# Kernel tuning notes

Hardware: AMD Instinct MI355X
Metric: run time of the kernel (lower is better)

## Reference

```python
import jax, jax.numpy as jnp
import numpy as np

V, D, H, L, T_CTX = 50257, 768, 12, 12, 1024
HD = D // H
GELU_C = float(np.sqrt(2.0 / np.pi))


def new_gelu(x):
    return 0.5 * x * (1.0 + jnp.tanh(GELU_C * (x + 0.044715 * x ** 3)))


def layernorm(x, w, b, eps=1e-5):
    mu = jnp.mean(x, axis=-1, keepdims=True)
    var = jnp.var(x, axis=-1, keepdims=True)
    return (x - mu) * jax.lax.rsqrt(var + eps) * w + b


def setup_inputs() -> dict:
    key = jax.random.key(0)
    ks = jax.random.split(key, 20)
    B, T = 2, 1024
    s = 0.02
    inp = {
        "idx": jax.random.randint(ks[0], (B, T), 0, V),
        "targets": jax.random.randint(ks[1], (B, T), 0, V),
        "wte": jax.random.normal(ks[2], (V, D), jnp.float32) * s,
        "wpe": jax.random.normal(ks[3], (T_CTX, D), jnp.float32) * s,
        "ln1_w": jnp.ones((L, D)), "ln1_b": jnp.zeros((L, D)),
        "qkv_w": jax.random.normal(ks[4], (L, D, 3 * D), jnp.float32) * s,
        "qkv_b": jnp.zeros((L, 3 * D)),
        "proj_w": jax.random.normal(ks[5], (L, D, D), jnp.float32) * s,
        "proj_b": jnp.zeros((L, D)),
        "ln2_w": jnp.ones((L, D)), "ln2_b": jnp.zeros((L, D)),
        "fc_w": jax.random.normal(ks[6], (L, D, 4 * D), jnp.float32) * s,
        "fc_b": jnp.zeros((L, 4 * D)),
        "fc2_w": jax.random.normal(ks[7], (L, 4 * D, D), jnp.float32) * s,
        "fc2_b": jnp.zeros((L, D)),
        "lnf_w": jnp.ones((D,)), "lnf_b": jnp.zeros((D,)),
    }
    return inp


def _gpt_forward(idx, targets, wte, wpe, ln1_w, ln1_b, qkv_w, qkv_b, proj_w,
                 proj_b, ln2_w, ln2_b, fc_w, fc_b, fc2_w, fc2_b, lnf_w, lnf_b):
    B, T = idx.shape
    x = wte[idx] + wpe[:T]  # [B,T,D]
    scale = 1.0 / np.sqrt(HD)
    causal = jnp.tril(jnp.ones((T, T), dtype=bool))

    def block(x, p):
        l1w, l1b, qw, qb, pw, pb, l2w, l2b, fw, fb, f2w, f2b = p
        h = layernorm(x, l1w, l1b)
        qkv = h @ qw + qb  # [B,T,3D]
        q, k, v = jnp.split(qkv, 3, axis=-1)
        q = q.reshape(B, T, H, HD).transpose(0, 2, 1, 3)
        k = k.reshape(B, T, H, HD).transpose(0, 2, 1, 3)
        v = v.reshape(B, T, H, HD).transpose(0, 2, 1, 3)
        attn = jnp.einsum('bhqd,bhkd->bhqk', q, k) * scale
        attn = jnp.where(causal, attn, -jnp.inf)
        attn = jax.nn.softmax(attn, axis=-1)
        o = jnp.einsum('bhqk,bhkd->bhqd', attn, v)
        o = o.transpose(0, 2, 1, 3).reshape(B, T, D)
        x = x + (o @ pw + pb)
        h = layernorm(x, l2w, l2b)
        h = new_gelu(h @ fw + fb) @ f2w + f2b
        return x + h, None

    params = (ln1_w, ln1_b, qkv_w, qkv_b, proj_w, proj_b,
              ln2_w, ln2_b, fc_w, fc_b, fc2_w, fc2_b)
    x, _ = jax.lax.scan(block, x, params)
    x = layernorm(x, lnf_w, lnf_b)
    logits = x @ wte.T  # tied lm_head, [B,T,V]

    logp = jax.nn.log_softmax(logits, axis=-1)
    tflat = targets.reshape(-1)
    valid = tflat != -1
    tsafe = jnp.where(valid, tflat, 0)
    nll = -jnp.take_along_axis(logp.reshape(-1, V), tsafe[:, None], axis=-1)[:, 0]
    loss = jnp.sum(jnp.where(valid, nll, 0.0)) / jnp.maximum(jnp.sum(valid), 1)
    return logits, loss


def reference(idx, targets, wte, wpe, ln1_w, ln1_b, qkv_w, qkv_b, proj_w,
              proj_b, ln2_w, ln2_b, fc_w, fc_b, fc2_w, fc2_b, lnf_w, lnf_b):
    return _gpt_forward(idx, targets, wte, wpe, ln1_w, ln1_b, qkv_w, qkv_b,
                        proj_w, proj_b, ln2_w, ln2_b, fc_w, fc_b, fc2_w, fc2_b,
                        lnf_w, lnf_b)
```

## Files before the change

kernel.cpp:

```cpp
#include <hip/hip_runtime.h>
#include <hip/hip_bf16.h>
#include <math.h>

#define TT 1024
#define BB 2
#define DD 768
#define HH 12
#define NHD 64
#define LL 12
#define VV 50257
#define MROWS (BB*TT)
#define VPAD 50304
#define NT 393

typedef __attribute__((ext_vector_type(4))) float f32x4;
typedef __attribute__((ext_vector_type(8))) __bf16 bf16x8;
typedef __attribute__((ext_vector_type(8))) unsigned short u16x8;
typedef __hip_bfloat16 bf16;

__device__ __forceinline__ void gload_lds16(const bf16* g, bf16* l) {
    __builtin_amdgcn_global_load_lds((const __attribute__((address_space(1))) void*)g,
                                     (__attribute__((address_space(3))) void*)l, 16, 0, 0);
}

__global__ void embed_kernel(const int* __restrict__ idx, const float* __restrict__ wte,
                             const float* __restrict__ wpe, float* __restrict__ x) {
    int m = blockIdx.x;
    int t = m % TT;
    int tok = idx[m];
    const float* wrow = wte + (size_t)tok * DD;
    const float* prow = wpe + (size_t)t * DD;
    float* xrow = x + (size_t)m * DD;
    for (int c = threadIdx.x; c < DD; c += blockDim.x)
        xrow[c] = wrow[c] + prow[c];
}

__global__ void ln_kernel(const float* __restrict__ x, const float* __restrict__ w,
                          const float* __restrict__ b, bf16* __restrict__ out) {
    __shared__ float red[256];
    int m = blockIdx.x;
    int tid = threadIdx.x;
    const float* xr = x + (size_t)m * DD;
    float v0 = xr[tid], v1 = xr[tid + 256], v2 = xr[tid + 512];
    red[tid] = v0 + v1 + v2;
    __syncthreads();
    for (int s = 128; s > 0; s >>= 1) { if (tid < s) red[tid] += red[tid + s]; __syncthreads(); }
    float mu = red[0] * (1.0f / DD);
    __syncthreads();
    float d0 = v0 - mu, d1 = v1 - mu, d2 = v2 - mu;
    red[tid] = d0 * d0 + d1 * d1 + d2 * d2;
    __syncthreads();
    for (int s = 128; s > 0; s >>= 1) { if (tid < s) red[tid] += red[tid + s]; __syncthreads(); }
    float rstd = rsqrtf(red[0] * (1.0f / DD) + 1e-5f);
    bf16* orow = out + (size_t)m * DD;
    orow[tid]       = __float2bfloat16(d0 * rstd * w[tid]       + b[tid]);
    orow[tid + 256] = __float2bfloat16(d1 * rstd * w[tid + 256] + b[tid + 256]);
    orow[tid + 512] = __float2bfloat16(d2 * rstd * w[tid + 512] + b[tid + 512]);
}

__global__ void redln_kernel(const float* __restrict__ part, const float* __restrict__ bias,
                             const float* __restrict__ w, const float* __restrict__ b,
                             float* __restrict__ x, bf16* __restrict__ hb) {
    __shared__ float red[256];
    const size_t MN = (size_t)MROWS * DD;
    int m = blockIdx.x;
    int tid = threadIdx.x;
    float v[3];
    #pragma unroll
    for (int j = 0; j < 3; ++j) {
        int c = tid + j * 256;
        size_t i = (size_t)m * DD + c;
        v[j] = x[i] + part[i] + part[MN + i] + bias[c];
        x[i] = v[j];
    }
    red[tid] = v[0] + v[1] + v[2];
    __syncthreads();
    for (int s = 128; s > 0; s >>= 1) { if (tid < s) red[tid] += red[tid + s]; __syncthreads(); }
    float mu = red[0] * (1.0f / DD);
    __syncthreads();
    float d0 = v[0] - mu, d1 = v[1] - mu, d2 = v[2] - mu;
    red[tid] = d0 * d0 + d1 * d1 + d2 * d2;
    __syncthreads();
    for (int s = 128; s > 0; s >>= 1) { if (tid < s) red[tid] += red[tid + s]; __syncthreads(); }
    float rstd = rsqrtf(red[0] * (1.0f / DD) + 1e-5f);
    bf16* orow = hb + (size_t)m * DD;
    orow[tid]       = __float2bfloat16(d0 * rstd * w[tid]       + b[tid]);
    orow[tid + 256] = __float2bfloat16(d1 * rstd * w[tid + 256] + b[tid + 256]);
    orow[tid + 512] = __float2bfloat16(d2 * rstd * w[tid + 512] + b[tid + 512]);
}

__global__ void cast_kernel(const float* __restrict__ src, bf16* __restrict__ dst, int n4) {
    int stride = gridDim.x * blockDim.x;
    for (int i = blockIdx.x * blockDim.x + threadIdx.x; i < n4; i += stride) {
        float4 v = *(const float4*)(src + (size_t)i * 4);
        bf16* d = dst + (size_t)i * 4;
        d[0] = __float2bfloat16(v.x); d[1] = __float2bfloat16(v.y);
        d[2] = __float2bfloat16(v.z); d[3] = __float2bfloat16(v.w);
    }
}

__global__ void padzero_kernel(bf16* __restrict__ p, int n) {
    int i = blockIdx.x * 256 + threadIdx.x;
    if (i < n) p[i] = __float2bfloat16(0.f);
}

__global__ void tcast_kernel(const float* __restrict__ W, bf16* __restrict__ Wt,
                             int K, int N, size_t wstride, size_t tstride) {
    W  += (size_t)blockIdx.z * wstride;
    Wt += (size_t)blockIdx.z * tstride;
    __shared__ float t[32][33];
    int n0 = blockIdx.x * 32, k0 = blockIdx.y * 32;
    int c = threadIdx.x & 31, g = threadIdx.x >> 5;
    #pragma unroll
    for (int i = 0; i < 4; ++i) {
        int k = g * 4 + i;
        t[k][c] = W[(size_t)(k0 + k) * N + n0 + c];
    }
    __syncthreads();
    #pragma unroll
    for (int i = 0; i < 4; ++i) {
        int n = g * 4 + i;
        Wt[(size_t)(n0 + n) * K + k0 + c] = __float2bfloat16(t[c][n]);
    }
}

template<int BM, int BN, bool BIAS, bool GELU_, bool RES, bool OUTBF16, bool SPLITK>
__global__ __launch_bounds__(256, 3) void mgemm(
        const bf16* __restrict__ A, const bf16* __restrict__ Bm,
        const float* __restrict__ bias, const float* __restrict__ res,
        float* __restrict__ Cf, bf16* __restrict__ Cb, int M, int N, int K) {
    constexpr int WM = BM / 32, WN = BN / 32;
    constexpr int RA = BM / 64, RB = BN / 64;
    constexpr int NL = RA + RB;
    __shared__ __align__(16) bf16 As[2][BM * 32];
    __shared__ __align__(16) bf16 Bs[2][BN * 32];
    const int tid = threadIdx.x, lane = tid & 63, wid = tid >> 6;
    const int nbx = gridDim.x;
    const int nwg = nbx * gridDim.y;
    const int bidl = blockIdx.x + nbx * blockIdx.y;
    const int cpx = nwg >> 3;
    const int sw = (bidl & 7) * cpx + (bidl >> 3);
    const int m0 = (sw % nbx) * BM, n0 = (sw / nbx) * BN;
    const int wr = (wid >> 1) * (BM / 2), wc = (wid & 1) * (BN / 2);
    const int fr = lane & 15, fq = lane >> 4;

    const int Keff  = SPLITK ? (K >> 1) : K;
    const int kbase = SPLITK ? blockIdx.z * Keff : 0;
    if (SPLITK) Cf += (size_t)blockIdx.z * M * N;

    const int ksrc = ((lane & 3) ^ ((lane >> 3) & 3)) * 8;
    const bf16* gA = A  + (size_t)(m0 + wid * 16 + (lane >> 2)) * K + kbase + ksrc;
    const bf16* gB = Bm + (size_t)(n0 + wid * 16 + (lane >> 2)) * K + kbase + ksrc;
    bf16* lA = &As[0][0] + wid * 512 + lane * 8;
    bf16* lB = &Bs[0][0] + wid * 512 + lane * 8;
    const int kph = (fq ^ ((fr >> 1) & 3)) * 8;

    f32x4 acc[WM][WN] = {};
    const int nt = Keff / 32;

    #pragma unroll
    for (int i = 0; i < RA; ++i) gload_lds16(gA + (size_t)(i * 64) * K, lA + i * 2048);
    #pragma unroll
    for (int i = 0; i < RB; ++i) gload_lds16(gB + (size_t)(i * 64) * K, lB + i * 2048);

    for (int t = 0; t < nt; ++t) {
        const int cur = t & 1;
        if (t + 1 < nt) {
            const bf16* pA = gA + (t + 1) * 32;
            const bf16* pB = gB + (t + 1) * 32;
            bf16* dA = lA + (cur ^ 1) * (BM * 32);
            bf16* dB = lB + (cur ^ 1) * (BN * 32);
            #pragma unroll
            for (int i = 0; i < RA; ++i) gload_lds16(pA + (size_t)(i * 64) * K, dA + i * 2048);
            #pragma unroll
            for (int i = 0; i < RB; ++i) gload_lds16(pB + (size_t)(i * 64) * K, dB + i * 2048);
            asm volatile("s_waitcnt vmcnt(%0)" :: "i"(NL) : "memory");
        } else {
            asm volatile("s_waitcnt vmcnt(0)" ::: "memory");
        }
        __builtin_amdgcn_s_barrier();
        __builtin_amdgcn_sched_barrier(0);
        const bf16* abase = &As[cur][0];
        const bf16* bbase = &Bs[cur][0];
        bf16x8 af[WM], bq[WN];
        #pragma unroll
        for (int m = 0; m < WM; ++m)
            af[m] = *(const bf16x8*)(abase + (wr + m * 16 + fr) * 32 + kph);
        #pragma unroll
        for (int n = 0; n < WN; ++n)
            bq[n] = *(const bf16x8*)(bbase + (wc + n * 16 + fr) * 32 + kph);
        #pragma unroll
        for (int m = 0; m < WM; ++m)
            #pragma unroll
            for (int n = 0; n < WN; ++n)
                acc[m][n] = __builtin_amdgcn_mfma_f32_16x16x32_bf16(af[m], bq[n], acc[m][n], 0, 0, 0);
        __builtin_amdgcn_sched_barrier(0);
        __builtin_amdgcn_s_barrier();
    }

    #pragma unroll
    for (int m = 0; m < WM; ++m) {
        const int row = m0 + wr + m * 16 + fq * 4;
        #pragma unroll
        for (int n = 0; n < WN; ++n) {
            const int col = n0 + wc + n * 16 + fr;
            float bv = BIAS ? bias[col] : 0.f;
            #pragma unroll
            for (int r = 0; r < 4; ++r) {
                float v = acc[m][n][r] + bv;
                if (GELU_) {
                    float u = v;
                    float z = 1.5957691216057308f * (u + 0.044715f * u * u * u);
                    v = u / (1.0f + __expf(-z));
                }
                if (RES) v += res[(size_t)(row + r) * N + col];
                if (OUTBF16) Cb[(size_t)(row + r) * N + col] = __float2bfloat16(v);
                else         Cf[(size_t)(row + r) * N + col] = v;
            }
        }
    }
}

__global__ __launch_bounds__(256, 3) void mgemmL(
        const bf16* __restrict__ A, const bf16* __restrict__ Bm,
        float* __restrict__ Cf, float2* __restrict__ P, int N, int K) {
    constexpr int NL = 4;
    __shared__ __align__(16) bf16 As[2][128 * 32];
    __shared__ __align__(16) bf16 Bs[2][128 * 32];
    __shared__ float2 lbuf[4][64];
    const int tid = threadIdx.x, lane = tid & 63, wid = tid >> 6;
    const int nbx = gridDim.x;
    const int nwg = nbx * gridDim.y;
    const int bidl = blockIdx.x + nbx * blockIdx.y;
    const int cpx = nwg >> 3;
    const int sw = (bidl & 7) * cpx + (bidl >> 3);
    const int m0 = (sw % nbx) * 128, n0 = (sw / nbx) * 128;
    const int wr = (wid >> 1) * 64, wc = (wid & 1) * 64;
    const int fr = lane & 15, fq = lane >> 4;

    const int ksrc = ((lane & 3) ^ ((lane >> 3) & 3)) * 8;
    const bf16* gA = A  + (size_t)(m0 + wid * 16 + (lane >> 2)) * K + ksrc;
    const bf16* gB = Bm + (size_t)(n0 + wid * 16 + (lane >> 2)) * K + ksrc;
    bf16* lA = &As[0][0] + wid * 512 + lane * 8;
    bf16* lB = &Bs[0][0] + wid * 512 + lane * 8;
    const int kph = (fq ^ ((fr >> 1) & 3)) * 8;

    f32x4 acc[4][4] = {};
    const int nt = K / 32;

    #pragma unroll
    for (int i = 0; i < 2; ++i) gload_lds16(gA + (size_t)(i * 64) * K, lA + i * 2048);
    #pragma unroll
    for (int i = 0; i < 2; ++i) gload_lds16(gB + (size_t)(i * 64) * K, lB + i * 2048);

    for (int t = 0; t < nt; ++t) {
        const int cur = t & 1;
        if (t + 1 < nt) {
            const bf16* pA = gA + (t + 1) * 32;
            const bf16* pB = gB + (t + 1) * 32;
            bf16* dA = lA + (cur ^ 1) * (128 * 32);
            bf16* dB = lB + (cur ^ 1) * (128 * 32);
            #pragma unroll
            for (int i = 0; i < 2; ++i) gload_lds16(pA + (size_t)(i * 64) * K, dA + i * 2048);
            #pragma unroll
            for (int i = 0; i < 2; ++i) gload_lds16(pB + (size_t)(i * 64) * K, dB + i * 2048);
            asm volatile("s_waitcnt vmcnt(%0)" :: "i"(NL) : "memory");
        } else {
            asm volatile("s_waitcnt vmcnt(0)" ::: "memory");
        }
        __builtin_amdgcn_s_barrier();
        __builtin_amdgcn_sched_barrier(0);
        const bf16* abase = &As[cur][0];
        const bf16* bbase = &Bs[cur][0];
        bf16x8 af[4], bq[4];
        #pragma unroll
        for (int m = 0; m < 4; ++m)
            af[m] = *(const bf16x8*)(abase + (wr + m * 16 + fr) * 32 + kph);
        #pragma unroll
        for (int n = 0; n < 4; ++n)
            bq[n] = *(const bf16x8*)(bbase + (wc + n * 16 + fr) * 32 + kph);
        #pragma unroll
        for (int m = 0; m < 4; ++m)
            #pragma unroll
            for (int n = 0; n < 4; ++n)
                acc[m][n] = __builtin_amdgcn_mfma_f32_16x16x32_bf16(af[m], bq[n], acc[m][n], 0, 0, 0);
        __builtin_amdgcn_sched_barrier(0);
        __builtin_amdgcn_s_barrier();
    }

    #pragma unroll
    for (int m = 0; m < 4; ++m) {
        const int row = m0 + wr + m * 16 + fq * 4;
        #pragma unroll
        for (int n = 0; n < 4; ++n) {
            const int col = n0 + wc + n * 16 + fr;
            if (col < N) {
                #pragma unroll
                for (int r = 0; r < 4; ++r)
                    Cf[(size_t)(row + r) * N + col] = acc[m][n][r];
            }
        }
    }
    #pragma unroll
    for (int m = 0; m < 4; ++m) {
        #pragma unroll
        for (int r = 0; r < 4; ++r) {
            float mx = -1e30f;
            #pragma unroll
            for (int n = 0; n < 4; ++n) {
                int col = n0 + wc + n * 16 + fr;
                mx = fmaxf(mx, (col < N) ? acc[m][n][r] : -1e30f);
            }
            #pragma unroll
            for (int msk = 1; msk <= 8; msk <<= 1) mx = fmaxf(mx, __shfl_xor(mx, msk));
            float sm = 0.f;
            #pragma unroll
            for (int n = 0; n < 4; ++n) {
                int col = n0 + wc + n * 16 + fr;
                if (col < N) sm += __expf(acc[m][n][r] - mx);
            }
            #pragma unroll
            for (int msk = 1; msk <= 8; msk <<= 1) sm += __shfl_xor(sm, msk);
            if (fr == 0) lbuf[wid][m * 16 + fq * 4 + r] = make_float2(mx, sm);
        }
    }
    __syncthreads();
    if (tid < 128) {
        int half = tid >> 6, rl = tid & 63;
        float2 a = lbuf[half * 2][rl];
        float2 b = lbuf[half * 2 + 1][rl];
        float mc = fmaxf(a.x, b.x);
        float sc = a.y * __expf(a.x - mc) + b.y * __expf(b.x - mc);
        P[(size_t)(m0 + half * 64 + rl) * NT + (n0 >> 7)] = make_float2(mc, sc);
    }
}

__global__ __launch_bounds__(256) void attn3_kernel(const bf16* __restrict__ qkv,
                                                    bf16* __restrict__ out) {
    __shared__ bf16 Vt[64 * 64];
    __shared__ bf16 Ps[4][16 * 64];
    const int bid = blockIdx.x;
    const int q0 = (15 - (bid & 15)) * 64;
    const int h  = (bid / (TT / 64)) % HH;
    const int b  = bid / ((TT / 64) * HH);
    const int tid = threadIdx.x, lane = tid & 63, wid = tid >> 6;
    const int fr = lane & 15, fq = lane >> 4;
    const size_t rs = 3 * DD;

    bf16x8 qf[2];
    {
        const bf16* qb = qkv + (size_t)(b * TT + q0 + wid * 16 + fr) * rs + h * NHD;
        qf[0] = *(const bf16x8*)(qb + fq * 8);
        qf[1] = *(const bf16x8*)(qb + 32 + fq * 8);
    }
    float mrun[4] = {-1e30f, -1e30f, -1e30f, -1e30f};
    float lrun[4] = {0.f, 0.f, 0.f, 0.f};
    f32x4 o[4] = {};
    const int vrow = (tid & 31) * 2, kq = tid >> 5;
    const int ntile = q0 / 64 + 1;

    for (int jt = 0; jt < ntile; ++jt) {
        __syncthreads();
        {
            const u16x8* vb = (const u16x8*)(qkv + (size_t)(b * TT + jt * 64 + vrow) * rs + 2 * DD + h * NHD + kq * 8);
            u16x8 v0 = vb[0];
            u16x8 v1 = *(const u16x8*)((const bf16*)vb + rs);
            #pragma unroll
            for (int j = 0; j < 8; ++j) {
                int d = kq * 8 + j;
                int e = (d * 64 + vrow) ^ ((d & 7) << 3);
                *(unsigned int*)&Vt[e] = (unsigned int)v0[j] | ((unsigned int)v1[j] << 16);
            }
        }
        f32x4 s[4] = {};
        const bf16* kb = qkv + (size_t)(b * TT + jt * 64 + fr) * rs + DD + h * NHD;
        __builtin_amdgcn_s_setprio(1);
        #pragma unroll
        for (int n = 0; n < 4; ++n) {
            bf16x8 k0 = *(const bf16x8*)(kb + (size_t)(n * 16) * rs + fq * 8);
            bf16x8 k1 = *(const bf16x8*)(kb + (size_t)(n * 16) * rs + 32 + fq * 8);
            s[n] = __builtin_amdgcn_mfma_f32_16x16x32_bf16(qf[0], k0, s[n], 0, 0, 0);
            s[n] = __builtin_amdgcn_mfma_f32_16x16x32_bf16(qf[1], k1, s[n], 0, 0, 0);
        }
        __builtin_amdgcn_s_setprio(0);
        float mt[4] = {-1e30f, -1e30f, -1e30f, -1e30f};
        #pragma unroll
        for (int n = 0; n < 4; ++n) {
            int colg = jt * 64 + n * 16 + fr;
            #pragma unroll
            for (int r = 0; r < 4; ++r) {
                int rowg = q0 + wid * 16 + fq * 4 + r;
                float v = s[n][r] * 0.125f;
                if (colg > rowg) v = -1e30f;
                s[n][r] = v;
                mt[r] = fmaxf(mt[r], v);
            }
        }
        #pragma unroll
        for (int msk = 1; msk <= 8; msk <<= 1)
            #pragma unroll
            for (int r = 0; r < 4; ++r) mt[r] = fmaxf(mt[r], __shfl_xor(mt[r], msk));
        float sc[4], pt[4] = {0.f, 0.f, 0.f, 0.f};
        #pragma unroll
        for (int r = 0; r < 4; ++r) {
            float mn = fmaxf(mrun[r], mt[r]);
            sc[r] = __expf(mrun[r] - mn);
            mrun[r] = mn;
        }
        #pragma unroll
        for (int n = 0; n < 4; ++n)
            #pragma unroll
            for (int r = 0; r < 4; ++r) {
                float p = __expf(s[n][r] - mrun[r]);
                s[n][r] = p;
                pt[r] += p;
            }
        #pragma unroll
        for (int msk = 1; msk <= 8; msk <<= 1)
            #pragma unroll
            for (int r = 0; r < 4; ++r) pt[r] += __shfl_xor(pt[r], msk);
        #pragma unroll
        for (int r = 0; r < 4; ++r) lrun[r] = lrun[r] * sc[r] + pt[r];
        #pragma unroll
        for (int n2 = 0; n2 < 4; ++n2)
            #pragma unroll
            for (int r = 0; r < 4; ++r) o[n2][r] *= sc[r];
        #pragma unroll
        for (int n = 0; n < 4; ++n)
            #pragma unroll
            for (int r = 0; r < 4; ++r) {
                int row = fq * 4 + r;
                int e = (row * 64 + n * 16 + fr) ^ ((row & 7) << 3);
                Ps[wid][e] = __float2bfloat16(s[n][r]);
            }
        __syncthreads();
        __builtin_amdgcn_s_setprio(1);
        #pragma unroll
        for (int ks = 0; ks < 2; ++ks) {
            int pe = (fr * 64 + ks * 32 + fq * 8) ^ ((fr & 7) << 3);
            bf16x8 pa = *(const bf16x8*)&Ps[wid][pe];
            #pragma unroll
            for (int n2 = 0; n2 < 4; ++n2) {
                int d = n2 * 16 + fr;
                int ve = (d * 64 + ks * 32 + fq * 8) ^ ((d & 7) << 3);
                bf16x8 vv = *(const bf16x8*)&Vt[ve];
                o[n2] = __builtin_amdgcn_mfma_f32_16x16x32_bf16(pa, vv, o[n2], 0, 0, 0);
            }
        }
        __builtin_amdgcn_s_setprio(0);
    }
    #pragma unroll
    for (int r = 0; r < 4; ++r) {
        float inv = 1.f / lrun[r];
        bf16* op = out + (size_t)(b * TT + q0 + wid * 16 + fq * 4 + r) * DD + h * NHD;
        #pragma unroll
        for (int n2 = 0; n2 < 4; ++n2)
            op[n2 * 16 + fr] = __float2bfloat16(o[n2][r] * inv);
    }
}

__global__ void zero_kernel(float* p) { if (threadIdx.x == 0) p[0] = 0.f; }

__global__ void loss_finish(const float2* __restrict__ P, const float* __restrict__ logits,
                            const int* __restrict__ targets, float* __restrict__ acc) {
    __shared__ float rm[256], rs[256];
    int m = blockIdx.x;
    int tid = threadIdx.x;
    float mx = -1e30f, sm = 0.f;
    for (int i = tid; i < NT; i += 256) {
        float2 p = P[(size_t)m * NT + i];
        float nm = fmaxf(mx, p.x);
        sm = sm * __expf(mx - nm) + p.y * __expf(p.x - nm);
        mx = nm;
    }
    rm[tid] = mx; rs[tid] = sm;
    __syncthreads();
    for (int s = 128; s > 0; s >>= 1) {
        if (tid < s) {
            float m2 = rm[tid + s], s2 = rs[tid + s];
            float nm = fmaxf(rm[tid], m2);
            rs[tid] = rs[tid] * __expf(rm[tid] - nm) + s2 * __expf(m2 - nm);
            rm[tid] = nm;
        }
        __syncthreads();
    }
    if (tid == 0) {
        float lse = logf(rs[0]) + rm[0];
        atomicAdd(acc, lse - logits[(size_t)m * VV + targets[m]]);
    }
}

__global__ void loss_final(const float* __restrict__ acc, float* __restrict__ out) {
    if (threadIdx.x == 0) out[0] = acc[0] * (1.0f / (float)MROWS);
}

extern "C" void kernel_launch(void* const* d_in, const int* in_sizes, int n_in,
                              void* d_out, int out_size, void* d_ws, size_t ws_size,
                              hipStream_t stream) {
    const int*   idx     = (const int*)d_in[0];
    const int*   targets = (const int*)d_in[1];
    const float* wte     = (const float*)d_in[2];
    const float* wpe     = (const float*)d_in[3];
    const float* ln1_w   = (const float*)d_in[4];
    const float* ln1_b   = (const float*)d_in[5];
    const float* qkv_w   = (const float*)d_in[6];
    const float* qkv_b   = (const float*)d_in[7];
    const float* proj_w  = (const float*)d_in[8];
    const float* proj_b  = (const float*)d_in[9];
    const float* ln2_w   = (const float*)d_in[10];
    const float* ln2_b   = (const float*)d_in[11];
    const float* fc_w    = (const float*)d_in[12];
    const float* fc_b    = (const float*)d_in[13];
    const float* fc2_w   = (const float*)d_in[14];
    const float* fc2_b   = (const float*)d_in[15];
    const float* lnf_w   = (const float*)d_in[16];
    const float* lnf_b   = (const float*)d_in[17];

    float* logits = (float*)d_out;
    float* loss_out = logits + (size_t)MROWS * VV;

    const size_t LQ = (size_t)3 * DD * DD, LP = (size_t)DD * DD;
    const size_t LF = (size_t)4 * DD * DD, LF2 = (size_t)4 * DD * DD;
    const size_t LSTRIDE = LQ + LP + LF + LF2;

    float* x    = (float*)d_ws;
    float* lacc = x + (size_t)MROWS * DD;
    float* part = lacc + 16;
    bf16* qkvbuf = (bf16*)(part + (size_t)2 * MROWS * DD);
    bf16* hb   = qkvbuf + (size_t)MROWS * 3 * DD;
    bf16* ab   = hb + (size_t)MROWS * DD;
    bf16* gb   = ab + (size_t)MROWS * DD;
    bf16* wteb = gb + (size_t)MROWS * 4 * DD;
    bf16* wbase = wteb + (size_t)VPAD * DD;

    const size_t fixed_bytes = (size_t)((char*)wbase - (char*)d_ws);
    const bool hoist = ws_size >= fixed_bytes + sizeof(bf16) * LSTRIDE * LL;

    dim3 blk(256);
    cast_kernel<<<2048, blk, 0, stream>>>(wte, wteb, VV * DD / 4);
    padzero_kernel<<<((VPAD - VV) * DD + 255) / 256, blk, 0, stream>>>(
        wteb + (size_t)VV * DD, (VPAD - VV) * DD);
    embed_kernel<<<MROWS, blk, 0, stream>>>(idx, wte, wpe, x);

    if (hoist) {
        tcast_kernel<<<dim3(3 * DD / 32, DD / 32, LL), blk, 0, stream>>>(
            qkv_w, wbase, DD, 3 * DD, LQ, LSTRIDE);
        tcast_kernel<<<dim3(DD / 32, DD / 32, LL), blk, 0, stream>>>(
            proj_w, wbase + LQ, DD, DD, LP, LSTRIDE);
        tcast_kernel<<<dim3(4 * DD / 32, DD / 32, LL), blk, 0, stream>>>(
            fc_w, wbase + LQ + LP, DD, 4 * DD, LF, LSTRIDE);
        tcast_kernel<<<dim3(DD / 32, 4 * DD / 32, LL), blk, 0, stream>>>(
            fc2_w, wbase + LQ + LP + LF, 4 * DD, DD, LF2, LSTRIDE);
    }

    ln_kernel<<<MROWS, blk, 0, stream>>>(x, ln1_w, ln1_b, hb);

    for (int l = 0; l < LL; ++l) {
        bf16* wl = hoist ? wbase + (size_t)l * LSTRIDE : wbase;
        bf16* wQT = wl, *wPT = wl + LQ, *wFT = wl + LQ + LP, *wF2T = wl + LQ + LP + LF;
        if (!hoist) {
            tcast_kernel<<<dim3(3 * DD / 32, DD / 32, 1), blk, 0, stream>>>(qkv_w + (size_t)l * LQ, wQT, DD, 3 * DD, 0, 0);
            tcast_kernel<<<dim3(DD / 32, DD / 32, 1), blk, 0, stream>>>(proj_w + (size_t)l * LP, wPT, DD, DD, 0, 0);
            tcast_kernel<<<dim3(4 * DD / 32, DD / 32, 1), blk, 0, stream>>>(fc_w + (size_t)l * LF, wFT, DD, 4 * DD, 0, 0);
            tcast_kernel<<<dim3(DD / 32, 4 * DD / 32, 1), blk, 0, stream>>>(fc2_w + (size_t)l * LF2, wF2T, 4 * DD, DD, 0, 0);
        }

        mgemm<128, 64, true, false, false, true, false><<<dim3(MROWS / 128, 3 * DD / 64), blk, 0, stream>>>(
            hb, wQT, qkv_b + (size_t)l * 3 * DD, nullptr, nullptr, qkvbuf, MROWS, 3 * DD, DD);

        attn3_kernel<<<BB * HH * (TT / 64), blk, 0, stream>>>(qkvbuf, ab);

        mgemm<64, 64, false, false, false, false, true><<<dim3(MROWS / 64, DD / 64, 2), blk, 0, stream>>>(
            ab, wPT, nullptr, nullptr, part, nullptr, MROWS, DD, DD);
        redln_kernel<<<MROWS, blk, 0, stream>>>(part, proj_b + (size_t)l * DD,
            ln2_w + (size_t)l * DD, ln2_b + (size_t)l * DD, x, hb);

        mgemm<128, 64, true, true, false, true, false><<<dim3(MROWS / 128, 4 * DD / 64), blk, 0, stream>>>(
            hb, wFT, fc_b + (size_t)l * 4 * DD, nullptr, nullptr, gb, MROWS, 4 * DD, DD);

        mgemm<64, 64, false, false, false, false, true><<<dim3(MROWS / 64, DD / 64, 2), blk, 0, stream>>>(
            gb, wF2T, nullptr, nullptr, part, nullptr, MROWS, DD, 4 * DD);
        const float* nw = (l + 1 < LL) ? ln1_w + (size_t)(l + 1) * DD : lnf_w;
        const float* nb = (l + 1 < LL) ? ln1_b + (size_t)(l + 1) * DD : lnf_b;
        redln_kernel<<<MROWS, blk, 0, stream>>>(part, fc2_b + (size_t)l * DD, nw, nb, x, hb);
    }

    mgemmL<<<dim3(MROWS / 128, VPAD / 128), blk, 0, stream>>>(
        hb, wteb, logits, (float2*)part, VV, DD);

    zero_kernel<<<1, 64, 0, stream>>>(lacc);
    loss_finish<<<MROWS, blk, 0, stream>>>((const float2*)part, logits, targets, lacc);
    loss_final<<<1, 64, 0, stream>>>(lacc, loss_out);
}
```

Baseline: 2.369 ms.

## Double GEMM K-tile to 64 with new XOR swizzle for LDS staging

Raises the per-iteration K depth in the bf16 MFMA GEMM from 32 to 64, doubling the LDS buffers and the number of global-to-LDS loads per stage. The swizzle changes to an 8-way XOR on rows of 64 elements, and the compute loop runs two K sub-steps per barrier pair. This halves the number of barriers and waitcnt round trips per K, at the cost of twice the LDS footprint, which may lower occupancy under launch_bounds(256,3).

New measurement: 2.363 ms. About the same (-0.2%).

```diff
diff --git a/kernel.cpp b/kernel.cpp
--- a/kernel.cpp
+++ b/kernel.cpp
@@ -130,10 +130,10 @@
         const float* __restrict__ bias, const float* __restrict__ res,
         float* __restrict__ Cf, bf16* __restrict__ Cb, int M, int N, int K) {
     constexpr int WM = BM / 32, WN = BN / 32;
-    constexpr int RA = BM / 64, RB = BN / 64;
+    constexpr int RA = BM / 32, RB = BN / 32;
     constexpr int NL = RA + RB;
-    __shared__ __align__(16) bf16 As[2][BM * 32];
-    __shared__ __align__(16) bf16 Bs[2][BN * 32];
+    __shared__ __align__(16) bf16 As[2][BM * 64];
+    __shared__ __align__(16) bf16 Bs[2][BN * 64];
     const int tid = threadIdx.x, lane = tid & 63, wid = tid >> 6;
     const int nbx = gridDim.x;
     const int nwg = nbx * gridDim.y;
@@ -148,52 +148,54 @@
     const int kbase = SPLITK ? blockIdx.z * Keff : 0;
     if (SPLITK) Cf += (size_t)blockIdx.z * M * N;
 
-    const int ksrc = ((lane & 3) ^ ((lane >> 3) & 3)) * 8;
-    const bf16* gA = A  + (size_t)(m0 + wid * 16 + (lane >> 2)) * K + kbase + ksrc;
-    const bf16* gB = Bm + (size_t)(n0 + wid * 16 + (lane >> 2)) * K + kbase + ksrc;
-    bf16* lA = &As[0][0] + wid * 512 + lane * 8;
-    bf16* lB = &Bs[0][0] + wid * 512 + lane * 8;
-    const int kph = (fq ^ ((fr >> 1) & 3)) * 8;
-
+    const int srow = tid >> 3;
+    const int sk   = ((tid & 7) ^ (srow & 7)) * 8;
+    const bf16* gA = A  + (size_t)(m0 + srow) * K + kbase + sk;
+    const bf16* gB = Bm + (size_t)(n0 + srow) * K + kbase + sk;
+
+    const int nt = Keff / 64;
     f32x4 acc[WM][WN] = {};
-    const int nt = Keff / 32;
-
-    #pragma unroll
-    for (int i = 0; i < RA; ++i) gload_lds16(gA + (size_t)(i * 64) * K, lA + i * 2048);
-    #pragma unroll
-    for (int i = 0; i < RB; ++i) gload_lds16(gB + (size_t)(i * 64) * K, lB + i * 2048);
+
+    auto stage = [&](int t) {
+        bf16* dA = &As[t & 1][0] + tid * 8;
+        bf16* dB = &Bs[t & 1][0] + tid * 8;
+        const bf16* pA = gA + t * 64;
+        const bf16* pB = gB + t * 64;
+        #pragma unroll
+        for (int u = 0; u < RA; ++u) gload_lds16(pA + (size_t)(u * 32) * K, dA + u * 2048);
+        #pragma unroll
+        for (int u = 0; u < RB; ++u) gload_lds16(pB + (size_t)(u * 32) * K, dB + u * 2048);
+    };
+
+    stage(0);
 
     for (int t = 0; t < nt; ++t) {
-        const int cur = t & 1;
         if (t + 1 < nt) {
-            const bf16* pA = gA + (t + 1) * 32;
-            const bf16* pB = gB + (t + 1) * 32;
-            bf16* dA = lA + (cur ^ 1) * (BM * 32);
-            bf16* dB = lB + (cur ^ 1) * (BN * 32);
-            #pragma unroll
-            for (int i = 0; i < RA; ++i) gload_lds16(pA + (size_t)(i * 64) * K, dA + i * 2048);
-            #pragma unroll
-            for (int i = 0; i < RB; ++i) gload_lds16(pB + (size_t)(i * 64) * K, dB + i * 2048);
+            stage(t + 1);
             asm volatile("s_waitcnt vmcnt(%0)" :: "i"(NL) : "memory");
         } else {
             asm volatile("s_waitcnt vmcnt(0)" ::: "memory");
         }
         __builtin_amdgcn_s_barrier();
         __builtin_amdgcn_sched_barrier(0);
-        const bf16* abase = &As[cur][0];
-        const bf16* bbase = &Bs[cur][0];
-        bf16x8 af[WM], bq[WN];
-        #pragma unroll
-        for (int m = 0; m < WM; ++m)
-            af[m] = *(const bf16x8*)(abase + (wr + m * 16 + fr) * 32 + kph);
-        #pragma unroll
-        for (int n = 0; n < WN; ++n)
-            bq[n] = *(const bf16x8*)(bbase + (wc + n * 16 + fr) * 32 + kph);
-        #pragma unroll
-        for (int m = 0; m < WM; ++m)
+        const bf16* abase = &As[t & 1][0];
+        const bf16* bbase = &Bs[t & 1][0];
+        #pragma unroll
+        for (int ks = 0; ks < 2; ++ks) {
+            const int kp = ((ks * 4 + fq) ^ (fr & 7)) * 8;
+            bf16x8 af[WM], bq[WN];
+            #pragma unroll
+            for (int m = 0; m < WM; ++m)
+                af[m] = *(const bf16x8*)(abase + (wr + m * 16 + fr) * 64 + kp);
             #pragma unroll
             for (int n = 0; n < WN; ++n)
-                acc[m][n] = __builtin_amdgcn_mfma_f32_16x16x32_bf16(af[m], bq[n], acc[m][n], 0, 0, 0);
+                bq[n] = *(const bf16x8*)(bbase + (wc + n * 16 + fr) * 64 + kp);
+            #pragma unroll
+            for (int m = 0; m < WM; ++m)
+                #pragma unroll
+                for (int n = 0; n < WN; ++n)
+                    acc[m][n] = __builtin_amdgcn_mfma_f32_16x16x32_bf16(af[m], bq[n], acc[m][n], 0, 0, 0);
+        }
         __builtin_amdgcn_sched_barrier(0);
         __builtin_amdgcn_s_barrier();
     }
```
